# Optimization experiments

Hardware: AMD Instinct MI355X
Metric: run time of the kernel (lower is better)

Reference implementation:

```python
import jax, jax.numpy as jnp
import numpy as np

B, N, DH = 256, 32, 128      # batch, n_agents, per-agent hidden
E = 496                       # n_edges (fully connected over 32 agents)
DIM_IN = 2 * DH               # 256, MLP input (concat of two agent states)
DIM_HID = 256
A = 12                        # dim_act
R = 4                         # payoff_rank
DIM_OUT = 2 * R * A           # 96


def setup_inputs() -> dict:
    key = jax.random.key(0)
    ks = jax.random.split(key, 7)
    hidden_states_n = jax.random.normal(ks[0], (B, N, DH), dtype=jnp.float32)
    edges_from = jax.random.randint(ks[1], (E,), 0, N, dtype=jnp.int32).astype(jnp.int64)
    edges_to = jax.random.randint(ks[2], (E,), 0, N, dtype=jnp.int32).astype(jnp.int64)
    # torch.nn.Linear params: W [out, in], b [out]
    W1 = jax.random.normal(ks[3], (DIM_HID, DIM_IN), dtype=jnp.float32) * (1.0 / np.sqrt(DIM_IN))
    b1 = jnp.zeros((DIM_HID,), dtype=jnp.float32)
    W2 = jax.random.normal(ks[4], (DIM_OUT, DIM_HID), dtype=jnp.float32) * (1.0 / np.sqrt(DIM_HID))
    b2 = jnp.zeros((DIM_OUT,), dtype=jnp.float32)
    return {"hidden_states_n": hidden_states_n, "W1": W1, "b1": b1, "W2": W2,
            "b2": b2, "edges_from": edges_from, "edges_to": edges_to}


def reference(hidden_states_n, W1, b1, W2, b2, edges_from, edges_to):
    hf = hidden_states_n[:, edges_from]                     # [B, E, DH]
    ht = hidden_states_n[:, edges_to]                       # [B, E, DH]
    # stack of (from||to, to||from): [2, B, E, 2*DH]
    inp = jnp.stack([jnp.concatenate([hf, ht], axis=-1),
                     jnp.concatenate([ht, hf], axis=-1)], axis=0)
    h = jax.nn.relu(inp @ W1.T + b1)                        # [2, B, E, DIM_HID]
    p = h @ W2.T + b2                                       # [2, B, E, 2*R*A]
    p = p.reshape(2, B, E, R, 2, A)
    # low-rank outer product per rank, summed over ranks: [2, B, E, A, A]
    payoffs = jnp.einsum('sberi,sberj->sbeij', p[..., 0, :], p[..., 1, :])
    # second copy is transposed, then mean over the two directions
    return 0.5 * (payoffs[0] + jnp.swapaxes(payoffs[1], -1, -2))  # [B, E, A, A]
```

## Files before the change

### kernel.cpp

```cpp
#include <hip/hip_runtime.h>

typedef unsigned int uint;
typedef _Float16 f16;

typedef __attribute__((ext_vector_type(8))) _Float16 f16x8;
typedef __attribute__((ext_vector_type(2))) _Float16 f16x2;
typedef __attribute__((ext_vector_type(4))) float f32x4;

#define E_CNT 496

#define W2_STRIDE 152
#define W2_HALF_F16 (96 * W2_STRIDE)
#define W2_HALF_BYTES (W2_HALF_F16 * 2)
#define W2_CHUNKS 29

__device__ __forceinline__ uint pack2_f16(float lo, float hi) {
    union { f16x2 h; uint u; } r;
    r.h[0] = (_Float16)lo;
    r.h[1] = (_Float16)hi;
    return r.u;
}

__device__ __forceinline__ void load_lds16(const void* g, void* l) {
    __builtin_amdgcn_global_load_lds(
        (const __attribute__((address_space(1))) void*)g,
        (__attribute__((address_space(3))) void*)l, 16, 0, 0);
}

__global__ __launch_bounds__(256) void x_kernel(
    const float* __restrict__ hidden, const float* __restrict__ W1,
    const float* __restrict__ b1, f16* __restrict__ Xout,
    const float* __restrict__ W2, f16* __restrict__ w2h) {
    __shared__ __align__(16) float hs[64 * 132];

    const int tid = threadIdx.x;

    if (blockIdx.x == 512) {
        #pragma unroll
        for (int j = 0; j < 24; ++j) {
            int idx4 = tid + j * 256;
            int n = idx4 >> 6;
            int k = (idx4 & 63) << 2;
            int h = k >> 7;
            int kin = k & 127;
            float4 v = *(const float4*)&W2[n * 256 + k];
            uint2 o;
            o.x = pack2_f16(v.x, v.y);
            o.y = pack2_f16(v.z, v.w);
            *(uint2*)&w2h[h * W2_HALF_F16 + n * W2_STRIDE + kin] = o;
        }
        return;
    }

    const int rowblock = blockIdx.x >> 2;
    const int g = blockIdx.x & 3;
    const int ln = tid & 63;
    const int waveId = tid >> 6;
    const int quad = ln >> 4;
    const int l16 = ln & 15;
    const int row0 = rowblock * 64;

    union FU { uint u[4]; f16x8 v; };
    FU wf[2][4];
    float bh[2][4];
    #pragma unroll
    for (int nt = 0; nt < 2; ++nt) {
        const int t = (g * 4 + waveId) * 2 + nt;
        const int half = t >> 4;
        const int htile = t & 15;
        const float* wrow = W1 + (htile * 16 + l16) * 256 + half * 128 + quad * 8;
        #pragma unroll
        for (int kk = 0; kk < 4; ++kk) {
            float4 v0 = *(const float4*)(wrow + kk * 32);
            float4 v1 = *(const float4*)(wrow + kk * 32 + 4);
            wf[nt][kk].u[0] = pack2_f16(v0.x, v0.y);
            wf[nt][kk].u[1] = pack2_f16(v0.z, v0.w);
            wf[nt][kk].u[2] = pack2_f16(v1.x, v1.y);
            wf[nt][kk].u[3] = pack2_f16(v1.z, v1.w);
        }
        #pragma unroll
        for (int r = 0; r < 4; ++r)
            bh[nt][r] = 0.5f * b1[htile * 16 + quad * 4 + r];
    }

    {
        const float* src = hidden + row0 * 128;
        #pragma unroll
        for (int it = 0; it < 8; ++it) {
            int idx = it * 256 + tid;
            int r = idx >> 5;
            int c4 = idx & 31;
            float4 v = *(const float4*)(src + idx * 4);
            *(float4*)&hs[r * 132 + c4 * 4] = v;
        }
    }
    __syncthreads();

    #pragma unroll
    for (int ch = 0; ch < 4; ++ch) {
        FU hf[4];
        const float* hrow = &hs[(ch * 16 + l16) * 132 + quad * 8];
        #pragma unroll
        for (int kk = 0; kk < 4; ++kk) {
            float4 v0 = *(const float4*)(hrow + kk * 32);
            float4 v1 = *(const float4*)(hrow + kk * 32 + 4);
            hf[kk].u[0] = pack2_f16(v0.x, v0.y);
            hf[kk].u[1] = pack2_f16(v0.z, v0.w);
            hf[kk].u[2] = pack2_f16(v1.x, v1.y);
            hf[kk].u[3] = pack2_f16(v1.z, v1.w);
        }
        #pragma unroll
        for (int nt = 0; nt < 2; ++nt) {
            const int t = (g * 4 + waveId) * 2 + nt;
            const int half = t >> 4;
            const int htile = t & 15;
            f32x4 acc = (f32x4){0.f, 0.f, 0.f, 0.f};
            #pragma unroll
            for (int kk = 0; kk < 4; ++kk)
                acc = __builtin_amdgcn_mfma_f32_16x16x32_f16(wf[nt][kk].v, hf[kk].v, acc, 0, 0, 0);
            uint2 o;
            o.x = pack2_f16(acc[0] + bh[nt][0], acc[1] + bh[nt][1]);
            o.y = pack2_f16(acc[2] + bh[nt][2], acc[3] + bh[nt][3]);
            f16* dst = Xout + half * (8192 * 256)
                     + (row0 + ch * 16 + l16) * 256 + htile * 16 + quad * 4;
            *(uint2*)dst = o;
        }
    }
}

__global__ __launch_bounds__(256, 4) void gemm_payoff_kernel(
    const f16* __restrict__ X1, const f16* __restrict__ X2,
    const int* __restrict__ e_f, const int* __restrict__ e_t,
    const f16* __restrict__ w2g, const float* __restrict__ b2,
    float* __restrict__ out) {

    __shared__ __align__(16) unsigned char smem[32768];
    f16* w2s = (f16*)smem;

    const int tid = threadIdx.x;
    const int ln = tid & 63;
    const int waveId = tid >> 6;
    const int quad = ln >> 4;
    const int l16 = ln & 15;
    const int pl = l16 & 7;
    const int s = l16 >> 3;

    const int bx = blockIdx.x;
    const int lb = (bx & 7) * 248 + (bx >> 3);

    auto stageW2 = [&](int h) {
        const unsigned char* src = (const unsigned char*)w2g + h * W2_HALF_BYTES + ln * 16;
        #pragma unroll
        for (int j = 0; j < 8; ++j) {
            int i = waveId + j * 4;
            if (i < W2_CHUNKS)
                load_lds16(src + i * 1024, smem + i * 1024);
        }
    };

    stageW2(0);

    bool f64 = true, t64 = true;
    #pragma unroll
    for (int i = 0; i < 16; ++i) {
        if (e_f[2 * i + 1] != 0) f64 = false;
        if (e_t[2 * i + 1] != 0) t64 = false;
    }

    const int pairBase = lb * 64 + waveId * 16;
    const f16* px1[2];
    const f16* px2[2];
    #pragma unroll
    for (int mt = 0; mt < 2; ++mt) {
        int pair = pairBase + mt * 8 + pl;
        int b = pair / E_CNT;
        int e = pair - b * E_CNT;
        int f = f64 ? e_f[2 * e] : e_f[e];
        int t = t64 ? e_t[2 * e] : e_t[e];
        int n1 = s ? t : f;
        int n2 = s ? f : t;
        px1[mt] = X1 + ((b * 32 + n1) * 256 + quad * 8);
        px2[mt] = X2 + ((b * 32 + n2) * 256 + quad * 8);
    }

    f32x4 acc[2][6];
    #pragma unroll
    for (int mt = 0; mt < 2; ++mt)
        #pragma unroll
        for (int tt = 0; tt < 6; ++tt) acc[mt][tt] = (f32x4){0.f, 0.f, 0.f, 0.f};

    typedef union { uint4 q; f16x8 h; } XU;
    XU G1[2][2], G2[2][2];

    #pragma unroll
    for (int mt = 0; mt < 2; ++mt) {
        G1[0][mt].q = *(const uint4*)(px1[mt] + 0 * 32);
        G2[0][mt].q = *(const uint4*)(px2[mt] + 0 * 32);
        G1[1][mt].q = *(const uint4*)(px1[mt] + 1 * 32);
        G2[1][mt].q = *(const uint4*)(px2[mt] + 1 * 32);
    }

    const f16x8 zero8 = (f16x8){0, 0, 0, 0, 0, 0, 0, 0};

    __syncthreads();

    #pragma unroll
    for (int kk = 0; kk < 4; ++kk) {
        const int buf = kk & 1;
        f16x8 af[2];
        #pragma unroll
        for (int mt = 0; mt < 2; ++mt) {
            f16x8 sum = G1[buf][mt].h + G2[buf][mt].h;
            af[mt] = __builtin_elementwise_max(sum, zero8);
        }
        #pragma unroll
        for (int mt = 0; mt < 2; ++mt) {
            G1[buf][mt].q = *(const uint4*)(px1[mt] + (kk + 2) * 32);
            G2[buf][mt].q = *(const uint4*)(px2[mt] + (kk + 2) * 32);
        }
        #pragma unroll
        for (int tt = 0; tt < 6; ++tt) {
            f16x8 bf = *(const f16x8*)&w2s[(tt * 16 + l16) * W2_STRIDE + kk * 32 + quad * 8];
            acc[0][tt] = __builtin_amdgcn_mfma_f32_16x16x32_f16(af[0], bf, acc[0][tt], 0, 0, 0);
            acc[1][tt] = __builtin_amdgcn_mfma_f32_16x16x32_f16(af[1], bf, acc[1][tt], 0, 0, 0);
        }
    }

    __syncthreads();
    stageW2(1);
    __syncthreads();

    #pragma unroll
    for (int kk = 4; kk < 8; ++kk) {
        const int buf = kk & 1;
        f16x8 af[2];
        #pragma unroll
        for (int mt = 0; mt < 2; ++mt) {
            f16x8 sum = G1[buf][mt].h + G2[buf][mt].h;
            af[mt] = __builtin_elementwise_max(sum, zero8);
        }
        if (kk < 6) {
            #pragma unroll
            for (int mt = 0; mt < 2; ++mt) {
                G1[buf][mt].q = *(const uint4*)(px1[mt] + (kk + 2) * 32);
                G2[buf][mt].q = *(const uint4*)(px2[mt] + (kk + 2) * 32);
            }
        }
        #pragma unroll
        for (int tt = 0; tt < 6; ++tt) {
            f16x8 bf = *(const f16x8*)&w2s[(tt * 16 + l16) * W2_STRIDE + (kk - 4) * 32 + quad * 8];
            acc[0][tt] = __builtin_amdgcn_mfma_f32_16x16x32_f16(af[0], bf, acc[0][tt], 0, 0, 0);
            acc[1][tt] = __builtin_amdgcn_mfma_f32_16x16x32_f16(af[1], bf, acc[1][tt], 0, 0, 0);
        }
    }

    float b2v[6];
    #pragma unroll
    for (int tt = 0; tt < 6; ++tt) b2v[tt] = b2[tt * 16 + l16];

    int d6[6];
    float pscale[6];
    {
        const int s_ = quad >> 1;
        #pragma unroll
        for (int tt = 0; tt < 6; ++tt) {
            int n = tt * 16 + l16;
            int rr = n / 24;
            int rem = n - rr * 24;
            int c01 = (rem >= 12) ? 1 : 0;
            int a = rem - c01 * 12;
            int k8 = s_ * 4 + rr;
            int toL = (c01 == s_) ? 1 : 0;
            d6[tt] = (toL ? 0 : 1024) + (quad & 1) * 512 + a * 8 + k8;
            pscale[tt] = toL ? 0.5f : 1.0f;
        }
    }

    __syncthreads();

    f16* pw = (f16*)smem + waveId * 4096;
    #pragma unroll
    for (int mt = 0; mt < 2; ++mt) {
        f16* pm = pw + mt * 2048;
        #pragma unroll
        for (int tt = 0; tt < 6; ++tt) {
            #pragma unroll
            for (int r = 0; r < 4; ++r)
                pm[d6[tt] + r * 128] = (_Float16)((acc[mt][tt][r] + b2v[tt]) * pscale[tt]);
        }
        #pragma unroll
        for (int pp = 0; pp < 8; ++pp) {
            f16x8 afp = zero8, bfp = zero8;
            if (quad == 0) {
                afp = *(const f16x8*)&pm[pp * 128 + l16 * 8];
                bfp = *(const f16x8*)&pm[1024 + pp * 128 + l16 * 8];
            }
            f32x4 d = __builtin_amdgcn_mfma_f32_16x16x32_f16(
                afp, bfp, (f32x4){0.f, 0.f, 0.f, 0.f}, 0, 0, 0);
            if (l16 < 12 && quad < 3) {
                float* ob = out + (pairBase + mt * 8 + pp) * 144 + quad * 48 + l16;
                #pragma unroll
                for (int r = 0; r < 4; ++r) ob[r * 12] = d[r];
            }
        }
    }
}

extern "C" void kernel_launch(void* const* d_in, const int* in_sizes, int n_in,
                              void* d_out, int out_size, void* d_ws, size_t ws_size,
                              hipStream_t stream) {
    const float* hidden = (const float*)d_in[0];
    const float* W1 = (const float*)d_in[1];
    const float* b1 = (const float*)d_in[2];
    const float* W2 = (const float*)d_in[3];
    const float* b2 = (const float*)d_in[4];
    const int* e_f = (const int*)d_in[5];
    const int* e_t = (const int*)d_in[6];
    float* out = (float*)d_out;

    char* ws = (char*)d_ws;
    f16* X = (f16*)ws;
    f16* w2h = (f16*)(ws + 8 * 1024 * 1024);

    x_kernel<<<513, 256, 0, stream>>>(hidden, W1, b1, X, W2, w2h);
    gemm_payoff_kernel<<<1984, 256, 0, stream>>>(X, X + 8192 * 256, e_f, e_t, w2h, b2, out);
}
```

Before: 141.5 us.

## Process M-tiles sequentially, shrink LDS strides, vectorize payoff stores

The GEMM-payoff kernel now processes its two 8-pair M-tiles one after another instead of together, so only one set of accumulators is live at a time, and W2 is restaged into LDS for the second tile. The W2 and payoff-scratch strides shrink, cutting LDS from 32 KB to 26 KB, and the explicit 4-waves occupancy hint is dropped. The payoff MFMA operands are swapped so each lane writes a contiguous float4 instead of four strided scalar stores. In exchange it adds extra barriers and a second full W2 staging pass per block, and the two tiles' global loads no longer overlap.

```diff
diff --git a/kernel.cpp b/kernel.cpp
--- a/kernel.cpp
+++ b/kernel.cpp
@@ -9,10 +9,15 @@
 
 #define E_CNT 496
 
-#define W2_STRIDE 152
+#define W2_STRIDE 136
 #define W2_HALF_F16 (96 * W2_STRIDE)
 #define W2_HALF_BYTES (W2_HALF_F16 * 2)
-#define W2_CHUNKS 29
+#define W2_CHUNKS 26
+#define LDS_BYTES 26624
+
+#define PP_STRIDE 136
+#define V_OFF 1088
+#define PW_F16 2176
 
 __device__ __forceinline__ uint pack2_f16(float lo, float hi) {
     union { f16x2 h; uint u; } r;
@@ -128,13 +133,13 @@
     }
 }
 
-__global__ __launch_bounds__(256, 4) void gemm_payoff_kernel(
+__global__ __launch_bounds__(256) void gemm_payoff_kernel(
     const f16* __restrict__ X1, const f16* __restrict__ X2,
     const int* __restrict__ e_f, const int* __restrict__ e_t,
     const f16* __restrict__ w2g, const float* __restrict__ b2,
     float* __restrict__ out) {
 
-    __shared__ __align__(16) unsigned char smem[32768];
+    __shared__ __align__(16) unsigned char smem[LDS_BYTES];
     f16* w2s = (f16*)smem;
 
     const int tid = threadIdx.x;
@@ -151,7 +156,7 @@
     auto stageW2 = [&](int h) {
         const unsigned char* src = (const unsigned char*)w2g + h * W2_HALF_BYTES + ln * 16;
         #pragma unroll
-        for (int j = 0; j < 8; ++j) {
+        for (int j = 0; j < 7; ++j) {
             int i = waveId + j * 4;
             if (i < W2_CHUNKS)
                 load_lds16(src + i * 1024, smem + i * 1024);
@@ -183,83 +188,12 @@
         px2[mt] = X2 + ((b * 32 + n2) * 256 + quad * 8);
     }
 
-    f32x4 acc[2][6];
-    #pragma unroll
-    for (int mt = 0; mt < 2; ++mt)
-        #pragma unroll
-        for (int tt = 0; tt < 6; ++tt) acc[mt][tt] = (f32x4){0.f, 0.f, 0.f, 0.f};
-
-    typedef union { uint4 q; f16x8 h; } XU;
-    XU G1[2][2], G2[2][2];
-
-    #pragma unroll
-    for (int mt = 0; mt < 2; ++mt) {
-        G1[0][mt].q = *(const uint4*)(px1[mt] + 0 * 32);
-        G2[0][mt].q = *(const uint4*)(px2[mt] + 0 * 32);
-        G1[1][mt].q = *(const uint4*)(px1[mt] + 1 * 32);
-        G2[1][mt].q = *(const uint4*)(px2[mt] + 1 * 32);
-    }
-
-    const f16x8 zero8 = (f16x8){0, 0, 0, 0, 0, 0, 0, 0};
-
-    __syncthreads();
-
-    #pragma unroll
-    for (int kk = 0; kk < 4; ++kk) {
-        const int buf = kk & 1;
-        f16x8 af[2];
-        #pragma unroll
-        for (int mt = 0; mt < 2; ++mt) {
-            f16x8 sum = G1[buf][mt].h + G2[buf][mt].h;
-            af[mt] = __builtin_elementwise_max(sum, zero8);
-        }
-        #pragma unroll
-        for (int mt = 0; mt < 2; ++mt) {
-            G1[buf][mt].q = *(const uint4*)(px1[mt] + (kk + 2) * 32);
-            G2[buf][mt].q = *(const uint4*)(px2[mt] + (kk + 2) * 32);
-        }
-        #pragma unroll
-        for (int tt = 0; tt < 6; ++tt) {
-            f16x8 bf = *(const f16x8*)&w2s[(tt * 16 + l16) * W2_STRIDE + kk * 32 + quad * 8];
-            acc[0][tt] = __builtin_amdgcn_mfma_f32_16x16x32_f16(af[0], bf, acc[0][tt], 0, 0, 0);
-            acc[1][tt] = __builtin_amdgcn_mfma_f32_16x16x32_f16(af[1], bf, acc[1][tt], 0, 0, 0);
-        }
-    }
-
-    __syncthreads();
-    stageW2(1);
-    __syncthreads();
-
-    #pragma unroll
-    for (int kk = 4; kk < 8; ++kk) {
-        const int buf = kk & 1;
-        f16x8 af[2];
-        #pragma unroll
-        for (int mt = 0; mt < 2; ++mt) {
-            f16x8 sum = G1[buf][mt].h + G2[buf][mt].h;
-            af[mt] = __builtin_elementwise_max(sum, zero8);
-        }
-        if (kk < 6) {
-            #pragma unroll
-            for (int mt = 0; mt < 2; ++mt) {
-                G1[buf][mt].q = *(const uint4*)(px1[mt] + (kk + 2) * 32);
-                G2[buf][mt].q = *(const uint4*)(px2[mt] + (kk + 2) * 32);
-            }
-        }
-        #pragma unroll
-        for (int tt = 0; tt < 6; ++tt) {
-            f16x8 bf = *(const f16x8*)&w2s[(tt * 16 + l16) * W2_STRIDE + (kk - 4) * 32 + quad * 8];
-            acc[0][tt] = __builtin_amdgcn_mfma_f32_16x16x32_f16(af[0], bf, acc[0][tt], 0, 0, 0);
-            acc[1][tt] = __builtin_amdgcn_mfma_f32_16x16x32_f16(af[1], bf, acc[1][tt], 0, 0, 0);
-        }
-    }
-
     float b2v[6];
     #pragma unroll
     for (int tt = 0; tt < 6; ++tt) b2v[tt] = b2[tt * 16 + l16];
 
     int d6[6];
-    float pscale[6];
+    float psc[6];
     {
         const int s_ = quad >> 1;
         #pragma unroll
@@ -271,37 +205,91 @@
             int a = rem - c01 * 12;
             int k8 = s_ * 4 + rr;
             int toL = (c01 == s_) ? 1 : 0;
-            d6[tt] = (toL ? 0 : 1024) + (quad & 1) * 512 + a * 8 + k8;
-            pscale[tt] = toL ? 0.5f : 1.0f;
-        }
-    }
-
-    __syncthreads();
-
-    f16* pw = (f16*)smem + waveId * 4096;
+            d6[tt] = (toL ? 0 : V_OFF) + (quad & 1) * 4 * PP_STRIDE + a * 8 + k8;
+            psc[tt] = toL ? 0.5f : 1.0f;
+        }
+    }
+
+    const f16x8 zero8 = (f16x8){0, 0, 0, 0, 0, 0, 0, 0};
+    f16* pm = (f16*)smem + waveId * PW_F16;
+
+    typedef union { uint4 q; f16x8 h; } XU;
+
     #pragma unroll
     for (int mt = 0; mt < 2; ++mt) {
-        f16* pm = pw + mt * 2048;
+        f32x4 acc[6];
+        #pragma unroll
+        for (int tt = 0; tt < 6; ++tt) acc[tt] = (f32x4){0.f, 0.f, 0.f, 0.f};
+
+        XU G1[2], G2[2];
+        G1[0].q = *(const uint4*)(px1[mt] + 0 * 32);
+        G2[0].q = *(const uint4*)(px2[mt] + 0 * 32);
+        G1[1].q = *(const uint4*)(px1[mt] + 1 * 32);
+        G2[1].q = *(const uint4*)(px2[mt] + 1 * 32);
+
+        __syncthreads();
+
+        #pragma unroll
+        for (int kk = 0; kk < 4; ++kk) {
+            const int buf = kk & 1;
+            f16x8 sum = G1[buf].h + G2[buf].h;
+            f16x8 af = __builtin_elementwise_max(sum, zero8);
+            G1[buf].q = *(const uint4*)(px1[mt] + (kk + 2) * 32);
+            G2[buf].q = *(const uint4*)(px2[mt] + (kk + 2) * 32);
+            #pragma unroll
+            for (int tt = 0; tt < 6; ++tt) {
+                f16x8 bf = *(const f16x8*)&w2s[(tt * 16 + l16) * W2_STRIDE + kk * 32 + quad * 8];
+                acc[tt] = __builtin_amdgcn_mfma_f32_16x16x32_f16(af, bf, acc[tt], 0, 0, 0);
+            }
+        }
+
+        __syncthreads();
+        stageW2(1);
+        __syncthreads();
+
+        #pragma unroll
+        for (int kk = 4; kk < 8; ++kk) {
+            const int buf = kk & 1;
+            f16x8 sum = G1[buf].h + G2[buf].h;
+            f16x8 af = __builtin_elementwise_max(sum, zero8);
+            if (kk < 6) {
+                G1[buf].q = *(const uint4*)(px1[mt] + (kk + 2) * 32);
+                G2[buf].q = *(const uint4*)(px2[mt] + (kk + 2) * 32);
+            }
+            #pragma unroll
+            for (int tt = 0; tt < 6; ++tt) {
+                f16x8 bf = *(const f16x8*)&w2s[(tt * 16 + l16) * W2_STRIDE + (kk - 4) * 32 + quad * 8];
+                acc[tt] = __builtin_amdgcn_mfma_f32_16x16x32_f16(af, bf, acc[tt], 0, 0, 0);
+            }
+        }
+
+        __syncthreads();
+
         #pragma unroll
         for (int tt = 0; tt < 6; ++tt) {
             #pragma unroll
             for (int r = 0; r < 4; ++r)
-                pm[d6[tt] + r * 128] = (_Float16)((acc[mt][tt][r] + b2v[tt]) * pscale[tt]);
-        }
+                pm[d6[tt] + r * PP_STRIDE] = (_Float16)((acc[tt][r] + b2v[tt]) * psc[tt]);
+        }
+
         #pragma unroll
         for (int pp = 0; pp < 8; ++pp) {
             f16x8 afp = zero8, bfp = zero8;
             if (quad == 0) {
-                afp = *(const f16x8*)&pm[pp * 128 + l16 * 8];
-                bfp = *(const f16x8*)&pm[1024 + pp * 128 + l16 * 8];
+                afp = *(const f16x8*)&pm[V_OFF + pp * PP_STRIDE + l16 * 8];
+                bfp = *(const f16x8*)&pm[pp * PP_STRIDE + l16 * 8];
             }
             f32x4 d = __builtin_amdgcn_mfma_f32_16x16x32_f16(
                 afp, bfp, (f32x4){0.f, 0.f, 0.f, 0.f}, 0, 0, 0);
             if (l16 < 12 && quad < 3) {
-                float* ob = out + (pairBase + mt * 8 + pp) * 144 + quad * 48 + l16;
-                #pragma unroll
-                for (int r = 0; r < 4; ++r) ob[r * 12] = d[r];
-            }
+                float* ob = out + (pairBase + mt * 8 + pp) * 144 + l16 * 12 + quad * 4;
+                *(float4*)ob = make_float4(d[0], d[1], d[2], d[3]);
+            }
+        }
+
+        if (mt == 0) {
+            __syncthreads();
+            stageW2(0);
         }
     }
 }
```

Measured after the change: 136.4 us. 1.04x faster.
